# Optimization experiments

Hardware: AMD Instinct MI355X
Metric: run time of the kernel (lower is better)

The kernel has to match this reference:

```python
import jax, jax.numpy as jnp
import numpy as np

TEMP = 0.2
N_IT = 10
P = 1


def setup_inputs() -> dict:
    key = jax.random.key(0)
    N, M = 8192, 8192
    k1, _ = jax.random.split(key)
    cdist = jax.random.uniform(k1, (N, M), dtype=jnp.float32)
    A = jnp.ones((N,), dtype=jnp.float32) / N  # uniform source density
    B = jnp.ones((M,), dtype=jnp.float32) / M  # uniform target density
    return {"cdist": cdist, "A": A, "B": B}


def reference(cdist, A, B):
    N, M = cdist.shape
    # C = (cdist - cdist.min()) / cdist.std(); torch std is unbiased (ddof=1)
    C = (cdist - cdist.min()) / jnp.std(cdist, ddof=1)
    # p == 1 -> no power applied
    Q = jnp.exp(-C / TEMP)
    Q = Q / Q.sum()

    def body(i, carry):
        U, V = carry
        # T implicit as U[:,None] * Q * V; first iter T == Q since U=V=1
        T = U[:, None] * Q * V[None, :]
        V = V * (B / T.sum(axis=0))
        T = U[:, None] * Q * V[None, :]
        U = U * (A / T.sum(axis=1))
        return (U, V)

    U0 = jnp.ones((N,), dtype=cdist.dtype)
    V0 = jnp.ones((M,), dtype=cdist.dtype)
    U, V = jax.lax.fori_loop(0, N_IT, body, (U0, V0))
    T = U[:, None] * Q * V[None, :]
    return T
```

## Files before the change

kernel.cpp:

```cpp
#include <hip/hip_runtime.h>
#include <hip/hip_fp16.h>

#define TEMP_ 0.2
#define NITER 10

typedef _Float16 half_t;
struct __align__(8)  H4 { half_t h[4]; };
struct __align__(16) H8 { half_t h[8]; };

__device__ __forceinline__ float wsum(float v){
#pragma unroll
  for (int o = 32; o > 0; o >>= 1) v += __shfl_down(v, o, 64);
  return v;
}
__device__ __forceinline__ double wsumd(double v){
#pragma unroll
  for (int o = 32; o > 0; o >>= 1) v += __shfl_down(v, o, 64);
  return v;
}
__device__ __forceinline__ float wmin(float v){
#pragma unroll
  for (int o = 32; o > 0; o >>= 1) v = fminf(v, __shfl_down(v, o, 64));
  return v;
}

__device__ __forceinline__ unsigned fenc(float f){
  unsigned u = __float_as_uint(f);
  return (u & 0x80000000u) ? ~u : (u | 0x80000000u);
}
__device__ __forceinline__ float fdec(unsigned u){
  return (u & 0x80000000u) ? __uint_as_float(u & 0x7FFFFFFFu) : __uint_as_float(~u);
}

__device__ __forceinline__ void get_stats(const double* __restrict__ sums,
                                          const unsigned* __restrict__ minbits,
                                          long long NM, float& cmin, float& kscale){
  double s  = sums[0];
  double ss = sums[1];
  double mean = s / (double)NM;
  double var  = (ss - mean * s) / (double)(NM - 1);
  cmin  = fdec(*minbits);
  kscale = (float)(1.0 / (sqrt(var) * TEMP_));
}

__global__ void k_init(double* __restrict__ sums, double* __restrict__ Ssum,
                       unsigned* __restrict__ minbits, float* __restrict__ colsum, int M){
  int i = blockIdx.x * blockDim.x + threadIdx.x;
  if (i == 0){ sums[0] = 0.0; sums[1] = 0.0; *Ssum = 0.0; *minbits = 0xFFFFFFFFu; }
  if (i < M) colsum[i] = 0.f;
}

__global__ __launch_bounds__(256) void k_reduce(const float* __restrict__ cd, long long n4,
                                                double* __restrict__ sums,
                                                unsigned* __restrict__ minbits){
  const float4* c4 = (const float4*)cd;
  long long i0 = (long long)blockIdx.x * blockDim.x + threadIdx.x;
  long long stride = (long long)gridDim.x * blockDim.x;
  double s = 0.0, ss = 0.0;
  float  fs = 0.f, fss = 0.f;
  float  mn = __int_as_float(0x7F800000);
  int cnt = 0;
  for (long long i = i0; i < n4; i += stride){
    float4 v = c4[i];
    mn = fminf(mn, fminf(fminf(v.x, v.y), fminf(v.z, v.w)));
    fs  += (v.x + v.y) + (v.z + v.w);
    fss += v.x*v.x + v.y*v.y + v.z*v.z + v.w*v.w;
    if (++cnt == 8){ s += fs; ss += fss; fs = 0.f; fss = 0.f; cnt = 0; }
  }
  s += fs; ss += fss;
  s = wsumd(s); ss = wsumd(ss); mn = wmin(mn);
  __shared__ double lds[8];
  __shared__ float  ldm[4];
  int lane = threadIdx.x & 63, wid = threadIdx.x >> 6;
  if (lane == 0){ lds[wid] = s; lds[4 + wid] = ss; ldm[wid] = mn; }
  __syncthreads();
  if (threadIdx.x == 0){
    unsafeAtomicAdd(&sums[0], lds[0] + lds[1] + lds[2] + lds[3]);
    unsafeAtomicAdd(&sums[1], lds[4] + lds[5] + lds[6] + lds[7]);
    atomicMin(minbits, fenc(fminf(fminf(ldm[0], ldm[1]), fminf(ldm[2], ldm[3]))));
  }
}

__global__ __launch_bounds__(256) void k_expcol(const float* __restrict__ cd, half_t* __restrict__ E,
                                                const double* __restrict__ sums,
                                                const unsigned* __restrict__ minbits,
                                                float* __restrict__ colsum, double* __restrict__ Ssum,
                                                int N, int M){
  float cmin, kscale;
  get_stats(sums, minbits, (long long)N * M, cmin, kscale);
  int c0 = blockIdx.x * 1024 + threadIdx.x * 4;
  int r0 = blockIdx.y * 64;
  float a0 = 0.f, a1 = 0.f, a2 = 0.f, a3 = 0.f;
#pragma unroll 4
  for (int r = 0; r < 64; ++r){
    long long idx = (long long)(r0 + r) * M + c0;
    float4 v = *(const float4*)(cd + idx);
    float e0 = __expf((cmin - v.x) * kscale);
    float e1 = __expf((cmin - v.y) * kscale);
    float e2 = __expf((cmin - v.z) * kscale);
    float e3 = __expf((cmin - v.w) * kscale);
    H4 o; o.h[0] = (half_t)e0; o.h[1] = (half_t)e1; o.h[2] = (half_t)e2; o.h[3] = (half_t)e3;
    *(H4*)(E + idx) = o;
    a0 += e0; a1 += e1; a2 += e2; a3 += e3;
  }
  unsafeAtomicAdd(&colsum[c0 + 0], a0);
  unsafeAtomicAdd(&colsum[c0 + 1], a1);
  unsafeAtomicAdd(&colsum[c0 + 2], a2);
  unsafeAtomicAdd(&colsum[c0 + 3], a3);
  float tot = wsum((a0 + a1) + (a2 + a3));
  __shared__ float lt[4];
  int lane = threadIdx.x & 63, wid = threadIdx.x >> 6;
  if (lane == 0) lt[wid] = tot;
  __syncthreads();
  if (threadIdx.x == 0) unsafeAtomicAdd(Ssum, (double)(lt[0] + lt[1] + lt[2] + lt[3]));
}

__global__ void k_v(const float* __restrict__ B, const float* __restrict__ colsum,
                    const double* __restrict__ Ssum, float* __restrict__ v, int M){
  int j = blockIdx.x * blockDim.x + threadIdx.x;
  if (j < M) v[j] = (float)((double)B[j] * (*Ssum) / (double)colsum[j]);
}

__global__ __launch_bounds__(256) void k_row(const half_t* __restrict__ E, const float* __restrict__ v,
                                             float* __restrict__ rowsum, int M){
  int t = threadIdx.x;
  int r0 = blockIdx.x * 8;
  float vr[32];
#pragma unroll
  for (int k = 0; k < 4; ++k){
    int c = k * 2048 + t * 8;
    float4 a = *(const float4*)(v + c);
    float4 b = *(const float4*)(v + c + 4);
    vr[k*8+0] = a.x; vr[k*8+1] = a.y; vr[k*8+2] = a.z; vr[k*8+3] = a.w;
    vr[k*8+4] = b.x; vr[k*8+5] = b.y; vr[k*8+6] = b.z; vr[k*8+7] = b.w;
  }
  __shared__ float lds[4][8];
  int lane = t & 63, wid = t >> 6;
  for (int r = 0; r < 8; ++r){
    const half_t* Er = E + (long long)(r0 + r) * M;
    float p = 0.f;
#pragma unroll
    for (int k = 0; k < 4; ++k){
      H8 hh = *(const H8*)(Er + k * 2048 + t * 8);
      p += (float)hh.h[0]*vr[k*8+0] + (float)hh.h[1]*vr[k*8+1]
         + (float)hh.h[2]*vr[k*8+2] + (float)hh.h[3]*vr[k*8+3]
         + (float)hh.h[4]*vr[k*8+4] + (float)hh.h[5]*vr[k*8+5]
         + (float)hh.h[6]*vr[k*8+6] + (float)hh.h[7]*vr[k*8+7];
    }
    p = wsum(p);
    if (lane == 0) lds[wid][r] = p;
  }
  __syncthreads();
  if (t < 8) rowsum[r0 + t] = lds[0][t] + lds[1][t] + lds[2][t] + lds[3][t];
}

__global__ void k_u(const float* __restrict__ A, const float* __restrict__ rowsum,
                    const double* __restrict__ Ssum, float* __restrict__ u,
                    float* __restrict__ colsum, int N, int M){
  int i = blockIdx.x * blockDim.x + threadIdx.x;
  if (i < N) u[i] = (float)((double)A[i] * (*Ssum) / (double)rowsum[i]);
  if (i < M) colsum[i] = 0.f;
}

__global__ __launch_bounds__(256) void k_col(const half_t* __restrict__ E, const float* __restrict__ u,
                                             float* __restrict__ colsum, int M){
  int c0 = blockIdx.x * 1024 + threadIdx.x * 4;
  int r0 = blockIdx.y * 64;
  float a0 = 0.f, a1 = 0.f, a2 = 0.f, a3 = 0.f;
#pragma unroll 4
  for (int r = 0; r < 64; ++r){
    int row = r0 + r;
    float ur = u[row];
    H4 hh = *(const H4*)(E + (long long)row * M + c0);
    a0 += ur * (float)hh.h[0];
    a1 += ur * (float)hh.h[1];
    a2 += ur * (float)hh.h[2];
    a3 += ur * (float)hh.h[3];
  }
  unsafeAtomicAdd(&colsum[c0 + 0], a0);
  unsafeAtomicAdd(&colsum[c0 + 1], a1);
  unsafeAtomicAdd(&colsum[c0 + 2], a2);
  unsafeAtomicAdd(&colsum[c0 + 3], a3);
}

__global__ __launch_bounds__(256) void k_final(const float* __restrict__ cd,
                                               const float* __restrict__ u, const float* __restrict__ v,
                                               const double* __restrict__ sums,
                                               const unsigned* __restrict__ minbits,
                                               const double* __restrict__ Ssum,
                                               float* __restrict__ T, int N, int M){
  float cmin, kscale;
  get_stats(sums, minbits, (long long)N * M, cmin, kscale);
  float invS = (float)(1.0 / (*Ssum));
  int t = threadIdx.x;
  int r0 = blockIdx.x * 8;
  float vr[32];
#pragma unroll
  for (int k = 0; k < 4; ++k){
    int c = k * 2048 + t * 8;
    float4 a = *(const float4*)(v + c);
    float4 b = *(const float4*)(v + c + 4);
    vr[k*8+0] = a.x * invS; vr[k*8+1] = a.y * invS; vr[k*8+2] = a.z * invS; vr[k*8+3] = a.w * invS;
    vr[k*8+4] = b.x * invS; vr[k*8+5] = b.y * invS; vr[k*8+6] = b.z * invS; vr[k*8+7] = b.w * invS;
  }
  for (int r = 0; r < 8; ++r){
    int row = r0 + r;
    float ur = u[row];
#pragma unroll
    for (int k = 0; k < 4; ++k){
      long long idx = (long long)row * M + k * 2048 + t * 8;
      float4 a = *(const float4*)(cd + idx);
      float4 b = *(const float4*)(cd + idx + 4);
      float4 oa, ob;
      oa.x = ur * vr[k*8+0] * __expf((cmin - a.x) * kscale);
      oa.y = ur * vr[k*8+1] * __expf((cmin - a.y) * kscale);
      oa.z = ur * vr[k*8+2] * __expf((cmin - a.z) * kscale);
      oa.w = ur * vr[k*8+3] * __expf((cmin - a.w) * kscale);
      ob.x = ur * vr[k*8+4] * __expf((cmin - b.x) * kscale);
      ob.y = ur * vr[k*8+5] * __expf((cmin - b.y) * kscale);
      ob.z = ur * vr[k*8+6] * __expf((cmin - b.z) * kscale);
      ob.w = ur * vr[k*8+7] * __expf((cmin - b.w) * kscale);
      *(float4*)(T + idx) = oa;
      *(float4*)(T + idx + 4) = ob;
    }
  }
}

extern "C" void kernel_launch(void* const* d_in, const int* in_sizes, int n_in,
                              void* d_out, int out_size, void* d_ws, size_t ws_size,
                              hipStream_t stream){
  const float* cd = (const float*)d_in[0];
  const float* A  = (const float*)d_in[1];
  const float* B  = (const float*)d_in[2];
  int N = in_sizes[1];
  int M = in_sizes[2];
  float*  T = (float*)d_out;
  half_t* E = (half_t*)d_out;

  char* ws = (char*)d_ws;
  double*   sums    = (double*)ws;
  double*   Ssum    = (double*)(ws + 16);
  unsigned* minbits = (unsigned*)(ws + 24);
  float*    colsum  = (float*)(ws + 32);
  float*    rowsum  = colsum + M;
  float*    u       = rowsum + N;
  float*    v       = u + N;

  int mx = (N > M) ? N : M;
  long long n4 = (long long)N * M / 4;

  k_init<<<(mx + 255) / 256, 256, 0, stream>>>(sums, Ssum, minbits, colsum, M);
  k_reduce<<<2048, 256, 0, stream>>>(cd, n4, sums, minbits);
  k_expcol<<<dim3(M / 1024, N / 64), 256, 0, stream>>>(cd, E, sums, minbits, colsum, Ssum, N, M);

  for (int it = 0; it < NITER; ++it){
    if (it > 0) k_col<<<dim3(M / 1024, N / 64), 256, 0, stream>>>(E, u, colsum, M);
    k_v<<<(M + 255) / 256, 256, 0, stream>>>(B, colsum, Ssum, v, M);
    k_row<<<N / 8, 256, 0, stream>>>(E, v, rowsum, M);
    k_u<<<(mx + 255) / 256, 256, 0, stream>>>(A, rowsum, Ssum, u, colsum, N, M);
  }
  k_final<<<N / 8, 256, 0, stream>>>(cd, u, v, sums, minbits, Ssum, T, N, M);
}
```

Before: 1.207 ms.

## Fuse entire Sinkhorn pipeline into one persistent cooperative kernel with grid syncs

Replaces the chain of about 40 separate kernel launches with a single persistent cooperative kernel that uses grid-wide barriers between phases. The u and v scaling vectors are now computed inline inside the row and column passes, with double-buffered column sums, so the small k_u/k_v kernels disappear. The final output is built from the stored fp16 exponentials rather than re-reading cdist and recomputing exp, and E moves into workspace instead of aliasing the output. This trades launch overhead and one full fp32 read for grid-sync costs and fp16 precision in the final T. The grid is capped by occupancy.

Result: slower. 2.332 ms (+93.2%).

```diff
diff --git a/kernel.cpp b/kernel.cpp
--- a/kernel.cpp
+++ b/kernel.cpp
@@ -1,5 +1,8 @@
 #include <hip/hip_runtime.h>
 #include <hip/hip_fp16.h>
+#include <hip/hip_cooperative_groups.h>
+
+namespace cg = cooperative_groups;
 
 #define TEMP_ 0.2
 #define NITER 10
@@ -32,196 +35,200 @@
   return (u & 0x80000000u) ? __uint_as_float(u & 0x7FFFFFFFu) : __uint_as_float(~u);
 }
 
-__device__ __forceinline__ void get_stats(const double* __restrict__ sums,
-                                          const unsigned* __restrict__ minbits,
-                                          long long NM, float& cmin, float& kscale){
-  double s  = sums[0];
-  double ss = sums[1];
-  double mean = s / (double)NM;
-  double var  = (ss - mean * s) / (double)(NM - 1);
-  cmin  = fdec(*minbits);
-  kscale = (float)(1.0 / (sqrt(var) * TEMP_));
-}
-
-__global__ void k_init(double* __restrict__ sums, double* __restrict__ Ssum,
-                       unsigned* __restrict__ minbits, float* __restrict__ colsum, int M){
-  int i = blockIdx.x * blockDim.x + threadIdx.x;
-  if (i == 0){ sums[0] = 0.0; sums[1] = 0.0; *Ssum = 0.0; *minbits = 0xFFFFFFFFu; }
-  if (i < M) colsum[i] = 0.f;
-}
-
-__global__ __launch_bounds__(256) void k_reduce(const float* __restrict__ cd, long long n4,
-                                                double* __restrict__ sums,
-                                                unsigned* __restrict__ minbits){
-  const float4* c4 = (const float4*)cd;
-  long long i0 = (long long)blockIdx.x * blockDim.x + threadIdx.x;
-  long long stride = (long long)gridDim.x * blockDim.x;
-  double s = 0.0, ss = 0.0;
-  float  fs = 0.f, fss = 0.f;
-  float  mn = __int_as_float(0x7F800000);
-  int cnt = 0;
-  for (long long i = i0; i < n4; i += stride){
-    float4 v = c4[i];
-    mn = fminf(mn, fminf(fminf(v.x, v.y), fminf(v.z, v.w)));
-    fs  += (v.x + v.y) + (v.z + v.w);
-    fss += v.x*v.x + v.y*v.y + v.z*v.z + v.w*v.w;
-    if (++cnt == 8){ s += fs; ss += fss; fs = 0.f; fss = 0.f; cnt = 0; }
-  }
-  s += fs; ss += fss;
-  s = wsumd(s); ss = wsumd(ss); mn = wmin(mn);
-  __shared__ double lds[8];
-  __shared__ float  ldm[4];
-  int lane = threadIdx.x & 63, wid = threadIdx.x >> 6;
-  if (lane == 0){ lds[wid] = s; lds[4 + wid] = ss; ldm[wid] = mn; }
-  __syncthreads();
-  if (threadIdx.x == 0){
-    unsafeAtomicAdd(&sums[0], lds[0] + lds[1] + lds[2] + lds[3]);
-    unsafeAtomicAdd(&sums[1], lds[4] + lds[5] + lds[6] + lds[7]);
-    atomicMin(minbits, fenc(fminf(fminf(ldm[0], ldm[1]), fminf(ldm[2], ldm[3]))));
-  }
-}
-
-__global__ __launch_bounds__(256) void k_expcol(const float* __restrict__ cd, half_t* __restrict__ E,
-                                                const double* __restrict__ sums,
-                                                const unsigned* __restrict__ minbits,
-                                                float* __restrict__ colsum, double* __restrict__ Ssum,
-                                                int N, int M){
+__global__ __launch_bounds__(256, 4) void sink_all(
+    const float* __restrict__ cd, const float* __restrict__ A, const float* __restrict__ B,
+    float* __restrict__ T, half_t* __restrict__ E,
+    double* __restrict__ sums, double* __restrict__ Ssum, unsigned* __restrict__ minbits,
+    float* __restrict__ csA, float* __restrict__ csB, float* __restrict__ rowsum,
+    int N, int M)
+{
+  cg::grid_group grid = cg::this_grid();
+  const int tid  = threadIdx.x;
+  const int lane = tid & 63, wid = tid >> 6;
+  const long long gtid     = (long long)blockIdx.x * 256 + tid;
+  const long long nthreads = (long long)gridDim.x * 256;
+
+  __shared__ double sd[8];
+  __shared__ float  sf[64];
+
+  for (long long i = gtid; i < M; i += nthreads){ csA[i] = 0.f; csB[i] = 0.f; }
+  if (gtid == 0){ sums[0] = 0.0; sums[1] = 0.0; *Ssum = 0.0; *minbits = 0xFFFFFFFFu; }
+  grid.sync();
+
+  {
+    const float4* c4 = (const float4*)cd;
+    long long n4 = (long long)N * M / 4;
+    double s = 0.0, ss = 0.0;
+    float fs = 0.f, fss = 0.f;
+    float mn = __int_as_float(0x7F800000);
+    int cnt = 0;
+    for (long long i = gtid; i < n4; i += nthreads){
+      float4 v = c4[i];
+      mn = fminf(mn, fminf(fminf(v.x, v.y), fminf(v.z, v.w)));
+      fs  += (v.x + v.y) + (v.z + v.w);
+      fss += v.x*v.x + v.y*v.y + v.z*v.z + v.w*v.w;
+      if (++cnt == 8){ s += fs; ss += fss; fs = 0.f; fss = 0.f; cnt = 0; }
+    }
+    s += fs; ss += fss;
+    s = wsumd(s); ss = wsumd(ss); mn = wmin(mn);
+    if (lane == 0){ sd[wid] = s; sd[4 + wid] = ss; sf[wid] = mn; }
+    __syncthreads();
+    if (tid == 0){
+      unsafeAtomicAdd(&sums[0], sd[0] + sd[1] + sd[2] + sd[3]);
+      unsafeAtomicAdd(&sums[1], sd[4] + sd[5] + sd[6] + sd[7]);
+      atomicMin(minbits, fenc(fminf(fminf(sf[0], sf[1]), fminf(sf[2], sf[3]))));
+    }
+    __syncthreads();
+  }
+  grid.sync();
+
   float cmin, kscale;
-  get_stats(sums, minbits, (long long)N * M, cmin, kscale);
-  int c0 = blockIdx.x * 1024 + threadIdx.x * 4;
-  int r0 = blockIdx.y * 64;
-  float a0 = 0.f, a1 = 0.f, a2 = 0.f, a3 = 0.f;
+  {
+    long long NM = (long long)N * M;
+    double s = sums[0], ss = sums[1];
+    double mean = s / (double)NM;
+    double var  = (ss - mean * s) / (double)(NM - 1);
+    cmin  = fdec(*minbits);
+    kscale = (float)(1.0 / (sqrt(var) * TEMP_));
+  }
+
+  const int TBX = M / 1024;
+  const int TB  = TBX * (N / 64);
+  const int NG  = N / 8;
+
+  for (int t = blockIdx.x; t < TB; t += gridDim.x){
+    int bx = t % TBX, by = t / TBX;
+    int c0 = bx * 1024 + tid * 4;
+    int r0 = by * 64;
+    float a0 = 0.f, a1 = 0.f, a2 = 0.f, a3 = 0.f;
 #pragma unroll 4
-  for (int r = 0; r < 64; ++r){
-    long long idx = (long long)(r0 + r) * M + c0;
-    float4 v = *(const float4*)(cd + idx);
-    float e0 = __expf((cmin - v.x) * kscale);
-    float e1 = __expf((cmin - v.y) * kscale);
-    float e2 = __expf((cmin - v.z) * kscale);
-    float e3 = __expf((cmin - v.w) * kscale);
-    H4 o; o.h[0] = (half_t)e0; o.h[1] = (half_t)e1; o.h[2] = (half_t)e2; o.h[3] = (half_t)e3;
-    *(H4*)(E + idx) = o;
-    a0 += e0; a1 += e1; a2 += e2; a3 += e3;
-  }
-  unsafeAtomicAdd(&colsum[c0 + 0], a0);
-  unsafeAtomicAdd(&colsum[c0 + 1], a1);
-  unsafeAtomicAdd(&colsum[c0 + 2], a2);
-  unsafeAtomicAdd(&colsum[c0 + 3], a3);
-  float tot = wsum((a0 + a1) + (a2 + a3));
-  __shared__ float lt[4];
-  int lane = threadIdx.x & 63, wid = threadIdx.x >> 6;
-  if (lane == 0) lt[wid] = tot;
-  __syncthreads();
-  if (threadIdx.x == 0) unsafeAtomicAdd(Ssum, (double)(lt[0] + lt[1] + lt[2] + lt[3]));
-}
-
-__global__ void k_v(const float* __restrict__ B, const float* __restrict__ colsum,
-                    const double* __restrict__ Ssum, float* __restrict__ v, int M){
-  int j = blockIdx.x * blockDim.x + threadIdx.x;
-  if (j < M) v[j] = (float)((double)B[j] * (*Ssum) / (double)colsum[j]);
-}
-
-__global__ __launch_bounds__(256) void k_row(const half_t* __restrict__ E, const float* __restrict__ v,
-                                             float* __restrict__ rowsum, int M){
-  int t = threadIdx.x;
-  int r0 = blockIdx.x * 8;
-  float vr[32];
-#pragma unroll
-  for (int k = 0; k < 4; ++k){
-    int c = k * 2048 + t * 8;
-    float4 a = *(const float4*)(v + c);
-    float4 b = *(const float4*)(v + c + 4);
-    vr[k*8+0] = a.x; vr[k*8+1] = a.y; vr[k*8+2] = a.z; vr[k*8+3] = a.w;
-    vr[k*8+4] = b.x; vr[k*8+5] = b.y; vr[k*8+6] = b.z; vr[k*8+7] = b.w;
-  }
-  __shared__ float lds[4][8];
-  int lane = t & 63, wid = t >> 6;
-  for (int r = 0; r < 8; ++r){
-    const half_t* Er = E + (long long)(r0 + r) * M;
-    float p = 0.f;
+    for (int r = 0; r < 64; ++r){
+      long long idx = (long long)(r0 + r) * M + c0;
+      float4 v = *(const float4*)(cd + idx);
+      float e0 = __expf((cmin - v.x) * kscale);
+      float e1 = __expf((cmin - v.y) * kscale);
+      float e2 = __expf((cmin - v.z) * kscale);
+      float e3 = __expf((cmin - v.w) * kscale);
+      H4 o; o.h[0] = (half_t)e0; o.h[1] = (half_t)e1; o.h[2] = (half_t)e2; o.h[3] = (half_t)e3;
+      *(H4*)(E + idx) = o;
+      a0 += e0; a1 += e1; a2 += e2; a3 += e3;
+    }
+    unsafeAtomicAdd(&csA[c0 + 0], a0);
+    unsafeAtomicAdd(&csA[c0 + 1], a1);
+    unsafeAtomicAdd(&csA[c0 + 2], a2);
+    unsafeAtomicAdd(&csA[c0 + 3], a3);
+    float tot = wsum((a0 + a1) + (a2 + a3));
+    __syncthreads();
+    if (lane == 0) sf[wid] = tot;
+    __syncthreads();
+    if (tid == 0) unsafeAtomicAdd(Ssum, (double)(sf[0] + sf[1] + sf[2] + sf[3]));
+  }
+  grid.sync();
+
+  const float Sf = (float)(*Ssum);
+
+  float* cur = csA;
+  float* nxt = csB;
+  for (int it = 0; it < NITER; ++it){
+    for (long long i = gtid; i < M; i += nthreads) nxt[i] = 0.f;
+
+    for (int g = blockIdx.x; g < NG; g += gridDim.x){
+      int r0 = g * 8;
+      float vr[32];
+#pragma unroll
+      for (int k = 0; k < 4; ++k){
+        int c = k * 2048 + tid * 8;
+        float4 a  = *(const float4*)(cur + c);
+        float4 b  = *(const float4*)(cur + c + 4);
+        float4 ba = *(const float4*)(B + c);
+        float4 bb = *(const float4*)(B + c + 4);
+        vr[k*8+0] = ba.x * Sf / a.x; vr[k*8+1] = ba.y * Sf / a.y;
+        vr[k*8+2] = ba.z * Sf / a.z; vr[k*8+3] = ba.w * Sf / a.w;
+        vr[k*8+4] = bb.x * Sf / b.x; vr[k*8+5] = bb.y * Sf / b.y;
+        vr[k*8+6] = bb.z * Sf / b.z; vr[k*8+7] = bb.w * Sf / b.w;
+      }
+      for (int r = 0; r < 8; ++r){
+        const half_t* Er = E + (long long)(r0 + r) * M;
+        float p = 0.f;
+#pragma unroll
+        for (int k = 0; k < 4; ++k){
+          H8 hh = *(const H8*)(Er + k * 2048 + tid * 8);
+          p += (float)hh.h[0]*vr[k*8+0] + (float)hh.h[1]*vr[k*8+1]
+             + (float)hh.h[2]*vr[k*8+2] + (float)hh.h[3]*vr[k*8+3]
+             + (float)hh.h[4]*vr[k*8+4] + (float)hh.h[5]*vr[k*8+5]
+             + (float)hh.h[6]*vr[k*8+6] + (float)hh.h[7]*vr[k*8+7];
+        }
+        p = wsum(p);
+        if (lane == 0) sf[wid * 8 + r] = p;
+      }
+      __syncthreads();
+      if (tid < 8) rowsum[r0 + tid] = sf[tid] + sf[8 + tid] + sf[16 + tid] + sf[24 + tid];
+      __syncthreads();
+    }
+    grid.sync();
+
+    if (it == NITER - 1) break;
+
+    for (int t = blockIdx.x; t < TB; t += gridDim.x){
+      int bx = t % TBX, by = t / TBX;
+      int r0 = by * 64;
+      __syncthreads();
+      if (tid < 64) sf[tid] = A[r0 + tid] * Sf / rowsum[r0 + tid];
+      __syncthreads();
+      int c0 = bx * 1024 + tid * 4;
+      float a0 = 0.f, a1 = 0.f, a2 = 0.f, a3 = 0.f;
+#pragma unroll 4
+      for (int r = 0; r < 64; ++r){
+        float ur = sf[r];
+        H4 hh = *(const H4*)(E + (long long)(r0 + r) * M + c0);
+        a0 += ur * (float)hh.h[0];
+        a1 += ur * (float)hh.h[1];
+        a2 += ur * (float)hh.h[2];
+        a3 += ur * (float)hh.h[3];
+      }
+      unsafeAtomicAdd(&nxt[c0 + 0], a0);
+      unsafeAtomicAdd(&nxt[c0 + 1], a1);
+      unsafeAtomicAdd(&nxt[c0 + 2], a2);
+      unsafeAtomicAdd(&nxt[c0 + 3], a3);
+    }
+    grid.sync();
+    float* tmp = cur; cur = nxt; nxt = tmp;
+  }
+
+  for (int g = blockIdx.x; g < NG; g += gridDim.x){
+    int r0 = g * 8;
+    float vr[32];
 #pragma unroll
     for (int k = 0; k < 4; ++k){
-      H8 hh = *(const H8*)(Er + k * 2048 + t * 8);
-      p += (float)hh.h[0]*vr[k*8+0] + (float)hh.h[1]*vr[k*8+1]
-         + (float)hh.h[2]*vr[k*8+2] + (float)hh.h[3]*vr[k*8+3]
-         + (float)hh.h[4]*vr[k*8+4] + (float)hh.h[5]*vr[k*8+5]
-         + (float)hh.h[6]*vr[k*8+6] + (float)hh.h[7]*vr[k*8+7];
-    }
-    p = wsum(p);
-    if (lane == 0) lds[wid][r] = p;
-  }
-  __syncthreads();
-  if (t < 8) rowsum[r0 + t] = lds[0][t] + lds[1][t] + lds[2][t] + lds[3][t];
-}
-
-__global__ void k_u(const float* __restrict__ A, const float* __restrict__ rowsum,
-                    const double* __restrict__ Ssum, float* __restrict__ u,
-                    float* __restrict__ colsum, int N, int M){
-  int i = blockIdx.x * blockDim.x + threadIdx.x;
-  if (i < N) u[i] = (float)((double)A[i] * (*Ssum) / (double)rowsum[i]);
-  if (i < M) colsum[i] = 0.f;
-}
-
-__global__ __launch_bounds__(256) void k_col(const half_t* __restrict__ E, const float* __restrict__ u,
-                                             float* __restrict__ colsum, int M){
-  int c0 = blockIdx.x * 1024 + threadIdx.x * 4;
-  int r0 = blockIdx.y * 64;
-  float a0 = 0.f, a1 = 0.f, a2 = 0.f, a3 = 0.f;
-#pragma unroll 4
-  for (int r = 0; r < 64; ++r){
-    int row = r0 + r;
-    float ur = u[row];
-    H4 hh = *(const H4*)(E + (long long)row * M + c0);
-    a0 += ur * (float)hh.h[0];
-    a1 += ur * (float)hh.h[1];
-    a2 += ur * (float)hh.h[2];
-    a3 += ur * (float)hh.h[3];
-  }
-  unsafeAtomicAdd(&colsum[c0 + 0], a0);
-  unsafeAtomicAdd(&colsum[c0 + 1], a1);
-  unsafeAtomicAdd(&colsum[c0 + 2], a2);
-  unsafeAtomicAdd(&colsum[c0 + 3], a3);
-}
-
-__global__ __launch_bounds__(256) void k_final(const float* __restrict__ cd,
-                                               const float* __restrict__ u, const float* __restrict__ v,
-                                               const double* __restrict__ sums,
-                                               const unsigned* __restrict__ minbits,
-                                               const double* __restrict__ Ssum,
-                                               float* __restrict__ T, int N, int M){
-  float cmin, kscale;
-  get_stats(sums, minbits, (long long)N * M, cmin, kscale);
-  float invS = (float)(1.0 / (*Ssum));
-  int t = threadIdx.x;
-  int r0 = blockIdx.x * 8;
-  float vr[32];
-#pragma unroll
-  for (int k = 0; k < 4; ++k){
-    int c = k * 2048 + t * 8;
-    float4 a = *(const float4*)(v + c);
-    float4 b = *(const float4*)(v + c + 4);
-    vr[k*8+0] = a.x * invS; vr[k*8+1] = a.y * invS; vr[k*8+2] = a.z * invS; vr[k*8+3] = a.w * invS;
-    vr[k*8+4] = b.x * invS; vr[k*8+5] = b.y * invS; vr[k*8+6] = b.z * invS; vr[k*8+7] = b.w * invS;
-  }
-  for (int r = 0; r < 8; ++r){
-    int row = r0 + r;
-    float ur = u[row];
-#pragma unroll
-    for (int k = 0; k < 4; ++k){
-      long long idx = (long long)row * M + k * 2048 + t * 8;
-      float4 a = *(const float4*)(cd + idx);
-      float4 b = *(const float4*)(cd + idx + 4);
-      float4 oa, ob;
-      oa.x = ur * vr[k*8+0] * __expf((cmin - a.x) * kscale);
-      oa.y = ur * vr[k*8+1] * __expf((cmin - a.y) * kscale);
-      oa.z = ur * vr[k*8+2] * __expf((cmin - a.z) * kscale);
-      oa.w = ur * vr[k*8+3] * __expf((cmin - a.w) * kscale);
-      ob.x = ur * vr[k*8+4] * __expf((cmin - b.x) * kscale);
-      ob.y = ur * vr[k*8+5] * __expf((cmin - b.y) * kscale);
-      ob.z = ur * vr[k*8+6] * __expf((cmin - b.z) * kscale);
-      ob.w = ur * vr[k*8+7] * __expf((cmin - b.w) * kscale);
-      *(float4*)(T + idx) = oa;
-      *(float4*)(T + idx + 4) = ob;
+      int c = k * 2048 + tid * 8;
+      float4 a  = *(const float4*)(cur + c);
+      float4 b  = *(const float4*)(cur + c + 4);
+      float4 ba = *(const float4*)(B + c);
+      float4 bb = *(const float4*)(B + c + 4);
+      vr[k*8+0] = ba.x * Sf / a.x; vr[k*8+1] = ba.y * Sf / a.y;
+      vr[k*8+2] = ba.z * Sf / a.z; vr[k*8+3] = ba.w * Sf / a.w;
+      vr[k*8+4] = bb.x * Sf / b.x; vr[k*8+5] = bb.y * Sf / b.y;
+      vr[k*8+6] = bb.z * Sf / b.z; vr[k*8+7] = bb.w * Sf / b.w;
+    }
+    for (int r = 0; r < 8; ++r){
+      int row = r0 + r;
+      float uf = A[row] / rowsum[row];
+#pragma unroll
+      for (int k = 0; k < 4; ++k){
+        long long idx = (long long)row * M + k * 2048 + tid * 8;
+        H8 hh = *(const H8*)(E + idx);
+        float4 oa, ob;
+        oa.x = uf * vr[k*8+0] * (float)hh.h[0];
+        oa.y = uf * vr[k*8+1] * (float)hh.h[1];
+        oa.z = uf * vr[k*8+2] * (float)hh.h[2];
+        oa.w = uf * vr[k*8+3] * (float)hh.h[3];
+        ob.x = uf * vr[k*8+4] * (float)hh.h[4];
+        ob.y = uf * vr[k*8+5] * (float)hh.h[5];
+        ob.z = uf * vr[k*8+6] * (float)hh.h[6];
+        ob.w = uf * vr[k*8+7] * (float)hh.h[7];
+        *(float4*)(T + idx)     = oa;
+        *(float4*)(T + idx + 4) = ob;
+      }
     }
   }
 }
@@ -234,30 +241,27 @@
   const float* B  = (const float*)d_in[2];
   int N = in_sizes[1];
   int M = in_sizes[2];
-  float*  T = (float*)d_out;
-  half_t* E = (half_t*)d_out;
+  float* T = (float*)d_out;
 
   char* ws = (char*)d_ws;
   double*   sums    = (double*)ws;
   double*   Ssum    = (double*)(ws + 16);
   unsigned* minbits = (unsigned*)(ws + 24);
-  float*    colsum  = (float*)(ws + 32);
-  float*    rowsum  = colsum + M;
-  float*    u       = rowsum + N;
-  float*    v       = u + N;
-
-  int mx = (N > M) ? N : M;
-  long long n4 = (long long)N * M / 4;
-
-  k_init<<<(mx + 255) / 256, 256, 0, stream>>>(sums, Ssum, minbits, colsum, M);
-  k_reduce<<<2048, 256, 0, stream>>>(cd, n4, sums, minbits);
-  k_expcol<<<dim3(M / 1024, N / 64), 256, 0, stream>>>(cd, E, sums, minbits, colsum, Ssum, N, M);
-
-  for (int it = 0; it < NITER; ++it){
-    if (it > 0) k_col<<<dim3(M / 1024, N / 64), 256, 0, stream>>>(E, u, colsum, M);
-    k_v<<<(M + 255) / 256, 256, 0, stream>>>(B, colsum, Ssum, v, M);
-    k_row<<<N / 8, 256, 0, stream>>>(E, v, rowsum, M);
-    k_u<<<(mx + 255) / 256, 256, 0, stream>>>(A, rowsum, Ssum, u, colsum, N, M);
-  }
-  k_final<<<N / 8, 256, 0, stream>>>(cd, u, v, sums, minbits, Ssum, T, N, M);
-}
+  float*    csA     = (float*)(ws + 64);
+  float*    csB     = csA + M;
+  float*    rowsum  = csB + M;
+  half_t*   E       = (half_t*)(ws + (1 << 20));
+
+  int occ = 4;
+  if (hipOccupancyMaxActiveBlocksPerMultiprocessor(&occ, sink_all, 256, 0) != hipSuccess || occ < 1)
+    occ = 4;
+  int G = occ * 256;
+  int maxG = N / 8;
+  if (G > maxG) G = maxG;
+
+  void* args[] = { (void*)&cd, (void*)&A, (void*)&B, (void*)&T, (void*)&E,
+                   (void*)&sums, (void*)&Ssum, (void*)&minbits,
+                   (void*)&csA, (void*)&csB, (void*)&rowsum,
+                   (void*)&N, (void*)&M };
+  hipLaunchCooperativeKernel((const void*)sink_all, dim3(G), dim3(256), args, 0, stream);
+}
```
